# Kernel optimization log

Measured on AMD Instinct MI355X. Metric: run time of the kernel, lower is better.

The kernel has to match this reference:

```python
import jax, jax.numpy as jnp
import numpy as np

EMBED = 1024
HEADS = 16
HDIM = 64
FF = 4096
N, S = 2, 2048
EPS = 1e-5


def _ln(x, g, b):
    m = jnp.mean(x, axis=-1, keepdims=True)
    v = jnp.mean((x - m) ** 2, axis=-1, keepdims=True)
    return (x - m) / jnp.sqrt(v + EPS) * g + b


def setup_inputs() -> dict:
    key = jax.random.key(0)
    ks = jax.random.split(key, 12)
    sd = 0.02
    inp = {
        'x': jax.random.normal(ks[0], (N, S, EMBED), dtype=jnp.float32),
        'mask': jnp.ones((N, 1, S, S), dtype=jnp.int32),
        'Wq': jax.random.normal(ks[1], (EMBED, HEADS * HDIM), dtype=jnp.float32) * sd,
        'bq': jnp.zeros((HEADS * HDIM,), dtype=jnp.float32),
        'Wk': jax.random.normal(ks[2], (EMBED, HEADS * HDIM), dtype=jnp.float32) * sd,
        'bk': jnp.zeros((HEADS * HDIM,), dtype=jnp.float32),
        'Wv': jax.random.normal(ks[3], (EMBED, HEADS * HDIM), dtype=jnp.float32) * sd,
        'bv': jnp.zeros((HEADS * HDIM,), dtype=jnp.float32),
        'Wo': jax.random.normal(ks[4], (HEADS * HDIM, EMBED), dtype=jnp.float32) * sd,
        'bo': jnp.zeros((EMBED,), dtype=jnp.float32),
        'g1': jnp.ones((EMBED,), dtype=jnp.float32),
        'beta1': jnp.zeros((EMBED,), dtype=jnp.float32),
        'g2': jnp.ones((EMBED,), dtype=jnp.float32),
        'beta2': jnp.zeros((EMBED,), dtype=jnp.float32),
        'W1': jax.random.normal(ks[5], (EMBED, FF), dtype=jnp.float32) * sd,
        'b1': jnp.zeros((FF,), dtype=jnp.float32),
        'W2': jax.random.normal(ks[6], (FF, EMBED), dtype=jnp.float32) * sd,
        'b2': jnp.zeros((EMBED,), dtype=jnp.float32),
    }
    return inp


def reference(x, mask, Wq, bq, Wk, bk, Wv, bv, Wo, bo, g1, beta1, g2, beta2, W1, b1, W2, b2):
    n, q_len, _ = x.shape
    # QKV projections, split into heads: [n, s, h, d]
    Q = (x @ Wq + bq).reshape(n, q_len, HEADS, HDIM)
    K = (x @ Wk + bk).reshape(n, q_len, HEADS, HDIM)
    V = (x @ Wv + bv).reshape(n, q_len, HEADS, HDIM)
    scores = jnp.einsum('nqhd,nkhd->nhqk', Q, K)
    scores = jnp.where(mask == 0, -jnp.inf, scores)
    # NOTE: original torch code is `attention / embed_size ** 1 / 2`,
    # which parses as (scores / embed_size) / 2 — replicated faithfully.
    attn = jax.nn.softmax(scores / EMBED / 2.0, axis=-1)
    ctx = jnp.einsum('nhqk,nkhd->nqhd', attn, V).reshape(n, q_len, HEADS * HDIM)
    proj = ctx @ Wo + bo
    h = _ln(proj + x, g1, beta1)  # dropout is identity (eval / p=0)
    ff = jax.nn.relu(h @ W1 + b1) @ W2 + b2
    out = _ln(ff + h, g2, beta2)
    return out
```

## Files before the change

### kernel.cpp

```cpp
#include <hip/hip_runtime.h>
#include <hip/hip_bf16.h>
#include <cstdint>
#include <cstddef>

#define EMBED 1024
#define SLEN  2048
#define NB    2
#define HEADS 16
#define HDIM  64
#define FFDIM 4096
#define ROWS  (NB * SLEN)
#define LOG2E 1.4426950408889634f

typedef __attribute__((ext_vector_type(8))) __bf16 bf16x8;
typedef __attribute__((ext_vector_type(4))) __bf16 bf16x4;
typedef __attribute__((ext_vector_type(4))) float  f32x4;

__device__ __forceinline__ void gload_lds16(const void* g, void* l) {
  __builtin_amdgcn_global_load_lds(
      (const __attribute__((address_space(1))) void*)g,
      (__attribute__((address_space(3))) void*)l, 16, 0, 0);
}

#define BAR()                              \
  do {                                     \
    __builtin_amdgcn_s_barrier();          \
    __builtin_amdgcn_sched_barrier(0);     \
  } while (0)
#define WAITVM(N)                                           \
  do {                                                      \
    asm volatile("s_waitcnt vmcnt(" #N ")" ::: "memory");   \
  } while (0)

__global__ __launch_bounds__(256) void cast_f32_bf16(const float* __restrict__ in,
                                                     __bf16* __restrict__ out, int n4) {
  int i = blockIdx.x * 256 + threadIdx.x;
  if (i >= n4) return;
  float4 v = ((const float4*)in)[i];
  bf16x4 o;
  o.x = (__bf16)v.x; o.y = (__bf16)v.y; o.z = (__bf16)v.z; o.w = (__bf16)v.w;
  ((bf16x4*)out)[i] = o;
}

__global__ __launch_bounds__(256) void transpose_all(
    const float* __restrict__ Wq, const float* __restrict__ Wk,
    const float* __restrict__ Wv, const float* __restrict__ Wo,
    const float* __restrict__ W1, const float* __restrict__ W2,
    __bf16* __restrict__ Wqt, __bf16* __restrict__ Wkt, __bf16* __restrict__ Wvt,
    __bf16* __restrict__ Wot, __bf16* __restrict__ W1t, __bf16* __restrict__ W2t) {
  __shared__ float t[64][65];
  const int b = blockIdx.x;
  const float* src;
  __bf16* dst;
  int R, C, tile;
  if (b < 1024) {
    const int w = b >> 8;
    tile = b & 255; R = 1024; C = 1024;
    src = (w == 0) ? Wq : (w == 1) ? Wk : (w == 2) ? Wv : Wo;
    dst = (w == 0) ? Wqt : (w == 1) ? Wkt : (w == 2) ? Wvt : Wot;
  } else if (b < 2048) {
    tile = b - 1024; R = 1024; C = 4096; src = W1; dst = W1t;
  } else {
    tile = b - 2048; R = 4096; C = 1024; src = W2; dst = W2t;
  }
  const int ct = C >> 6;
  const int tr = (tile / ct) * 64, tc = (tile % ct) * 64;
  const int tx = threadIdx.x & 63;
  const int ty = threadIdx.x >> 6;
#pragma unroll
  for (int i = 0; i < 16; ++i) {
    int a = ty * 16 + i;
    t[a][tx] = src[(size_t)(tr + a) * C + tc + tx];
  }
  __syncthreads();
#pragma unroll
  for (int i = 0; i < 16; ++i) {
    int bb = ty * 16 + i;
    dst[(size_t)(tc + bb) * R + tr + tx] = (__bf16)t[tx][bb];
  }
}

__global__ __launch_bounds__(256) void mask_flags_k(const int* __restrict__ mask,
                                                    int* __restrict__ flags) {
  const int b = blockIdx.x;
  const int kt = b & 31, qt = (b >> 5) & 15, n = b >> 9;
  const int tid = threadIdx.x;
  const int* base = mask + ((size_t)n * SLEN + qt * 128) * SLEN + kt * 64;
  const int rw = tid >> 4;
  const int cg = tid & 15;
  int ok = 1;
#pragma unroll
  for (int i = 0; i < 8; ++i) {
    int4 v = ((const int4*)(base + (size_t)(rw + i * 16) * SLEN))[cg];
    ok &= (v.x != 0) & (v.y != 0) & (v.z != 0) & (v.w != 0);
  }
  __shared__ int red;
  if (tid == 0) red = 1;
  __syncthreads();
  if (!ok) red = 0;
  __syncthreads();
  if (tid == 0) flags[b] = red;
}

template <int MODE>
__global__ __launch_bounds__(512, 1) void gemm256(
    const __bf16* __restrict__ A, const __bf16* __restrict__ Bt,
    const float* __restrict__ bias, const float* __restrict__ bias2,
    const float* __restrict__ bias3,
    void* __restrict__ outp, void* __restrict__ outp2, void* __restrict__ outp3,
    int M, int N, int K, int Kc, float oscale) {
  __shared__ __align__(16) char smem[69632];
  const int tid = threadIdx.x;
  const int lane = tid & 63;
  const int ntile = N >> 8;
  const int mt = M >> 8;
  const int cpx = gridDim.x >> 3;
  int u = (blockIdx.x & 7) * cpx + (blockIdx.x >> 3);
  int kz = 0;
  if constexpr (MODE == 5) {
    const int tiles = mt * ntile;
    kz = u / tiles;
    u -= kz * tiles;
  }
  int bm, bn;
  {
    const int G = (ntile >= 4) ? 4 : ntile;
    const int gsz = mt * G;
    const int g = u / gsz;
    const int rem = u - g * gsz;
    bm = rem / G;
    bn = g * G + rem % G;
  }
  const int trow = bm << 8, tcol = bn << 8;

  const int r0 = tid & 255;
  const int c0 = tid >> 8;
  const __bf16* Ag = A + (size_t)(trow + r0) * K + (size_t)kz * Kc + c0 * 8;
  const __bf16* Bg = Bt + (size_t)(tcol + r0) * K + (size_t)kz * Kc + c0 * 8;

  auto stage = [&](int buf, int kt) {
    const __bf16* a0 = Ag + (size_t)kt * 32;
    const __bf16* b0 = Bg + (size_t)kt * 32;
    char* la = smem + buf * 32768 + tid * 16;
    char* lb = la + 16384;
    gload_lds16(a0, la);
    gload_lds16(a0 + 16, la + 8192);
    gload_lds16(b0, lb);
    gload_lds16(b0 + 16, lb + 8192);
  };

  const int wave = tid >> 6;
  const int wr = wave >> 2;
  const int wc = wave & 3;
  const int l16 = lane & 15;
  const int g4 = lane >> 4;

  f32x4 acc[8][4];
#pragma unroll
  for (int i = 0; i < 8; ++i)
#pragma unroll
    for (int j = 0; j < 4; ++j) acc[i][j] = (f32x4)0.0f;

  const int nk = Kc >> 5;
  stage(0, 0);
  stage(1, 1);
  WAITVM(4);
  BAR();
  int cur = 0;
  for (int kt = 0; kt < nk; ++kt) {
    bf16x8 af[8], bfr[4];
#pragma unroll
    for (int i = 0; i < 8; ++i)
      af[i] = *(const bf16x8*)(smem + cur * 32768 + g4 * 4096 +
                               (wr * 128 + i * 16 + l16) * 16);
#pragma unroll
    for (int j = 0; j < 4; ++j)
      bfr[j] = *(const bf16x8*)(smem + cur * 32768 + 16384 + g4 * 4096 +
                                (wc * 64 + j * 16 + l16) * 16);
#pragma unroll
    for (int mi = 0; mi < 8; ++mi)
#pragma unroll
      for (int ni = 0; ni < 4; ++ni)
        acc[mi][ni] =
            __builtin_amdgcn_mfma_f32_16x16x32_bf16(af[mi], bfr[ni], acc[mi][ni], 0, 0, 0);
    BAR();
    if (kt + 2 < nk) {
      stage(cur, kt + 2);
      WAITVM(4);
    } else {
      WAITVM(0);
    }
    BAR();
    cur ^= 1;
  }

  if constexpr (MODE == 5) {
#pragma unroll
    for (int mi = 0; mi < 8; ++mi)
#pragma unroll
      for (int ni = 0; ni < 4; ++ni) {
        const int col = tcol + wc * 64 + ni * 16 + l16;
#pragma unroll
        for (int r = 0; r < 4; ++r) {
          const int row = trow + wr * 128 + mi * 16 + g4 * 4 + r;
          ((float*)outp)[(size_t)kz * M * N + (size_t)row * N + col] = acc[mi][ni][r];
        }
      }
  } else {
    const int sel = (MODE == 4) ? (tcol >> 10) : 0;
    const float* bp = (MODE == 4) ? (sel == 0 ? bias : sel == 1 ? bias2 : bias3) : bias;
    const int cc0 = (MODE == 4) ? (tcol & 1023) : tcol;
    const int n = trow >> 11;
    if (MODE == 4 && sel == 2) {
      __bf16(*repT)[136] = (__bf16(*)[136])smem;
#pragma unroll
      for (int h = 0; h < 2; ++h) {
        __syncthreads();
        if (wr == h) {
#pragma unroll
          for (int mi = 0; mi < 8; ++mi)
#pragma unroll
            for (int ni = 0; ni < 4; ++ni) {
              const int cl = wc * 64 + ni * 16 + l16;
              const float bcol = bp[cc0 + cl];
#pragma unroll
              for (int r = 0; r < 4; ++r)
                repT[cl][mi * 16 + g4 * 4 + r] = (__bf16)(acc[mi][ni][r] + bcol);
            }
        }
        __syncthreads();
#pragma unroll
        for (int it = 0; it < 8; ++it) {
          const int cidx = it * 512 + tid;
          const int cl = cidx >> 4, seg = cidx & 15;
          const int col = cc0 + cl, hh = col >> 6, dd = col & 63;
          *(bf16x8*)((__bf16*)outp3 + ((size_t)((n * HEADS + hh) * HDIM) + dd) * SLEN +
                     (trow & 2047) + h * 128 + seg * 8) = *(const bf16x8*)&repT[cl][seg * 8];
        }
      }
    } else {
      __bf16(*rep)[264] = (__bf16(*)[264])smem;
#pragma unroll
      for (int h = 0; h < 2; ++h) {
        __syncthreads();
        if (wr == h) {
#pragma unroll
          for (int mi = 0; mi < 8; ++mi)
#pragma unroll
            for (int ni = 0; ni < 4; ++ni) {
              const int cl = wc * 64 + ni * 16 + l16;
              float bcol = bp[cc0 + cl];
#pragma unroll
              for (int r = 0; r < 4; ++r) {
                float v = acc[mi][ni][r] + bcol;
                if constexpr (MODE == 4) {
                  if (sel == 0) v *= oscale;
                } else {
                  v = fmaxf(v, 0.0f);
                }
                rep[mi * 16 + g4 * 4 + r][cl] = (__bf16)v;
              }
            }
        }
        __syncthreads();
        if constexpr (MODE == 3) {
#pragma unroll
          for (int it = 0; it < 8; ++it) {
            const int cidx = it * 512 + tid;
            const int rl = cidx >> 5, seg = cidx & 31;
            *(bf16x8*)((__bf16*)outp + (size_t)(trow + h * 128 + rl) * N + tcol + seg * 8) =
                *(const bf16x8*)&rep[rl][seg * 8];
          }
        } else {
          __bf16* dst = (sel == 0) ? (__bf16*)outp : (__bf16*)outp2;
#pragma unroll
          for (int it = 0; it < 8; ++it) {
            const int cidx = it * 512 + tid;
            const int rl = cidx >> 5, seg = cidx & 31;
            const int col = cc0 + seg * 8, hh = col >> 6, d = col & 63;
            const int s = (trow & 2047) + h * 128 + rl;
            *(bf16x8*)(dst + ((size_t)((n * HEADS + hh) * SLEN) + s) * HDIM + d) =
                *(const bf16x8*)&rep[rl][seg * 8];
          }
        }
      }
    }
  }
}

__global__ __launch_bounds__(256, 2) void gemm_bt5(
    const __bf16* __restrict__ A, const __bf16* __restrict__ Bt,
    float* __restrict__ outp, int M, int N, int K, int Kc) {
  __shared__ __align__(16) char smem[32768];
  const int tid = threadIdx.x;
  const int lane = tid & 63;
  const int ntile = N >> 7;
  const int cpx = gridDim.x >> 3;
  int u = (blockIdx.x & 7) * cpx + (blockIdx.x >> 3);
  const int tiles = (M >> 7) * ntile;
  const int kz = u / tiles;
  u -= kz * tiles;
  const int bm = u / ntile;
  const int bn = u % ntile;
  const int trow = bm << 7;
  const int tcol = bn << 7;

  const int c0 = tid >> 7;
  const int r0 = tid & 127;
  const __bf16* Ag = A + (size_t)(trow + r0) * K + (size_t)kz * Kc + c0 * 8;
  const __bf16* Bg = Bt + (size_t)(tcol + r0) * K + (size_t)kz * Kc + c0 * 8;

  auto stage = [&](int buf, int kt) {
    const __bf16* a0 = Ag + (size_t)kt * 32;
    const __bf16* b0 = Bg + (size_t)kt * 32;
    char* la = smem + buf * 16384 + tid * 16;
    char* lb = la + 8192;
    gload_lds16(a0, la);
    gload_lds16(a0 + 16, la + 4096);
    gload_lds16(b0, lb);
    gload_lds16(b0 + 16, lb + 4096);
  };

  const int wave = tid >> 6;
  const int wr = (wave >> 1) * 64;
  const int wc = (wave & 1) * 64;
  const int l16 = lane & 15;
  const int g4 = lane >> 4;

  f32x4 acc[4][4];
#pragma unroll
  for (int i = 0; i < 4; ++i)
#pragma unroll
    for (int j = 0; j < 4; ++j) acc[i][j] = (f32x4)0.0f;

  const int nk = Kc >> 5;
  stage(0, 0);
  stage(1, 1);
  WAITVM(4);
  BAR();
  int cur = 0;
  for (int kt = 0; kt < nk; ++kt) {
    bf16x8 af[4], bfr[4];
#pragma unroll
    for (int i = 0; i < 4; ++i) {
      af[i]  = *(const bf16x8*)(smem + cur * 16384 + g4 * 2048 + (wr + i * 16 + l16) * 16);
      bfr[i] = *(const bf16x8*)(smem + cur * 16384 + 8192 + g4 * 2048 + (wc + i * 16 + l16) * 16);
    }
#pragma unroll
    for (int mi = 0; mi < 4; ++mi)
#pragma unroll
      for (int ni = 0; ni < 4; ++ni)
        acc[mi][ni] =
            __builtin_amdgcn_mfma_f32_16x16x32_bf16(af[mi], bfr[ni], acc[mi][ni], 0, 0, 0);
    BAR();
    if (kt + 2 < nk) {
      stage(cur, kt + 2);
      WAITVM(4);
    } else {
      WAITVM(0);
    }
    BAR();
    cur ^= 1;
  }
#pragma unroll
  for (int mi = 0; mi < 4; ++mi)
#pragma unroll
    for (int ni = 0; ni < 4; ++ni) {
      const int col = tcol + wc + ni * 16 + l16;
#pragma unroll
      for (int r = 0; r < 4; ++r) {
        const int row = trow + wr + mi * 16 + g4 * 4 + r;
        outp[(size_t)kz * M * N + (size_t)row * N + col] = acc[mi][ni][r];
      }
    }
}

__global__ __launch_bounds__(256, 3) void attn_k(const __bf16* __restrict__ Q,
                                                 const __bf16* __restrict__ K,
                                                 const __bf16* __restrict__ Vt,
                                                 const int* __restrict__ mask,
                                                 const int* __restrict__ flags,
                                                 __bf16* __restrict__ ctx) {
  const int tid = threadIdx.x, lane = tid & 63, wave = tid >> 6;
  const int l16 = lane & 15, g4 = lane >> 4;
  const int bid = blockIdx.x;
  const int lb = (bid & 7) * 64 + (bid >> 3);
  const int qt = lb & 15, h = (lb >> 4) & 15, n = lb >> 8;
  const int q0 = qt * 128 + wave * 32;
  const __bf16* Qh = Q + (size_t)(n * HEADS + h) * SLEN * HDIM;
  const __bf16* Kh = K + (size_t)(n * HEADS + h) * SLEN * HDIM;
  const __bf16* Vh = Vt + (size_t)(n * HEADS + h) * HDIM * SLEN;
  const int* Mh = mask + (size_t)n * SLEN * SLEN;
  const int* Fh = flags + (n * 16 + qt) * 32;

  __shared__ __bf16 KV[2][2][8][64][8];
  __shared__ __align__(16) __bf16 P_lds[4][2][16][72];

  const int srow = tid & 63;
  const int schunk = tid >> 6;
  const __bf16* Kg = Kh + (size_t)srow * HDIM + schunk * 8;
  const __bf16* Vg = Vh + (size_t)srow * SLEN + schunk * 8;
  auto stage = [&](int buf, int kb) {
    char* lk = (char*)&KV[buf][0][0][0][0] + tid * 16;
    char* lv = (char*)&KV[buf][1][0][0][0] + tid * 16;
    const __bf16* kg = Kg + (size_t)kb * 64 * HDIM;
    const __bf16* vg = Vg + kb * 64;
    gload_lds16(kg, lk);
    gload_lds16(kg + 32, lk + 4096);
    gload_lds16(vg, lv);
    gload_lds16(vg + 32, lv + 4096);
  };

  const unsigned long long fbits = __ballot(Fh[lane & 31] != 0);

  bf16x8 qf[2][2];
#pragma unroll
  for (int mq = 0; mq < 2; ++mq)
#pragma unroll
    for (int kd = 0; kd < 2; ++kd)
      qf[mq][kd] =
          *(const bf16x8*)(Qh + (size_t)(q0 + mq * 16 + l16) * HDIM + kd * 32 + g4 * 8);

  float m_[2], lsum[2];
  f32x4 o[2][4];
#pragma unroll
  for (int mq = 0; mq < 2; ++mq) {
    m_[mq] = -INFINITY;
    lsum[mq] = 0.0f;
#pragma unroll
    for (int ni = 0; ni < 4; ++ni) o[mq][ni] = (f32x4)0.0f;
  }

  const int nt = SLEN / 64;
  stage(0, 0);
  stage(1, 1);
  WAITVM(4);
  BAR();
  int cur = 0;
  for (int kt = 0; kt < nt; ++kt) {
    const int kbase = kt * 64;
    const bool full = (fbits >> kt) & 1ull;
    f32x4 s[2][4];
#pragma unroll
    for (int mq = 0; mq < 2; ++mq)
#pragma unroll
      for (int ni = 0; ni < 4; ++ni) s[mq][ni] = (f32x4)0.0f;
    __builtin_amdgcn_s_setprio(1);
#pragma unroll
    for (int ni = 0; ni < 4; ++ni) {
      bf16x8 kf0 = *(const bf16x8*)&KV[cur][0][g4][ni * 16 + l16][0];
      bf16x8 kf1 = *(const bf16x8*)&KV[cur][0][4 + g4][ni * 16 + l16][0];
#pragma unroll
      for (int mq = 0; mq < 2; ++mq) {
        s[mq][ni] = __builtin_amdgcn_mfma_f32_16x16x32_bf16(kf0, qf[mq][0], s[mq][ni], 0, 0, 0);
        s[mq][ni] = __builtin_amdgcn_mfma_f32_16x16x32_bf16(kf1, qf[mq][1], s[mq][ni], 0, 0, 0);
      }
    }
    __builtin_amdgcn_s_setprio(0);
    if (!full) {
#pragma unroll
      for (int mq = 0; mq < 2; ++mq)
#pragma unroll
        for (int ni = 0; ni < 4; ++ni)
#pragma unroll
          for (int r = 0; r < 4; ++r) {
            const int mk =
                Mh[(size_t)(q0 + mq * 16 + l16) * SLEN + kbase + ni * 16 + 4 * g4 + r];
            s[mq][ni][r] = mk ? s[mq][ni][r] : -INFINITY;
          }
    }
    float pmax[2];
#pragma unroll
    for (int mq = 0; mq < 2; ++mq) {
      float a = fmaxf(fmaxf(s[mq][0][0], s[mq][0][1]), fmaxf(s[mq][0][2], s[mq][0][3]));
      float b = fmaxf(fmaxf(s[mq][1][0], s[mq][1][1]), fmaxf(s[mq][1][2], s[mq][1][3]));
      float c = fmaxf(fmaxf(s[mq][2][0], s[mq][2][1]), fmaxf(s[mq][2][2], s[mq][2][3]));
      float d = fmaxf(fmaxf(s[mq][3][0], s[mq][3][1]), fmaxf(s[mq][3][2], s[mq][3][3]));
      pmax[mq] = fmaxf(fmaxf(a, b), fmaxf(c, d));
    }
    const int ok = (pmax[0] <= m_[0] + 8.0f) & (pmax[1] <= m_[1] + 8.0f);
    if (!__all(ok)) {
#pragma unroll
      for (int mq = 0; mq < 2; ++mq) {
        float pm = fmaxf(m_[mq], pmax[mq]);
        pm = fmaxf(pm, __shfl_xor(pm, 16));
        pm = fmaxf(pm, __shfl_xor(pm, 32));
        const float al = __builtin_amdgcn_exp2f(m_[mq] - pm);
        m_[mq] = pm;
        lsum[mq] *= al;
#pragma unroll
        for (int r = 0; r < 4; ++r) {
          const float ao = __shfl(al, 4 * g4 + r);
#pragma unroll
          for (int ni = 0; ni < 4; ++ni) o[mq][ni][r] *= ao;
        }
      }
    }
#pragma unroll
    for (int mq = 0; mq < 2; ++mq) {
      float ls = 0.0f;
#pragma unroll
      for (int ni = 0; ni < 4; ++ni) {
        bf16x4 pk;
#pragma unroll
        for (int r = 0; r < 4; ++r) {
          const float p = __builtin_amdgcn_exp2f(s[mq][ni][r] - m_[mq]);
          ls += p;
          pk[r] = (__bf16)p;
        }
        *(bf16x4*)&P_lds[wave][mq][l16][ni * 16 + 4 * g4] = pk;
      }
      lsum[mq] += ls;
    }
    __builtin_amdgcn_s_setprio(1);
#pragma unroll
    for (int kb = 0; kb < 2; ++kb) {
      bf16x8 pa0 = *(const bf16x8*)&P_lds[wave][0][l16][kb * 32 + 8 * g4];
      bf16x8 pa1 = *(const bf16x8*)&P_lds[wave][1][l16][kb * 32 + 8 * g4];
#pragma unroll
      for (int ni = 0; ni < 4; ++ni) {
        bf16x8 vf = *(const bf16x8*)&KV[cur][1][kb * 4 + g4][ni * 16 + l16][0];
        o[0][ni] = __builtin_amdgcn_mfma_f32_16x16x32_bf16(pa0, vf, o[0][ni], 0, 0, 0);
        o[1][ni] = __builtin_amdgcn_mfma_f32_16x16x32_bf16(pa1, vf, o[1][ni], 0, 0, 0);
      }
    }
    __builtin_amdgcn_s_setprio(0);
    BAR();
    if (kt + 2 < nt) {
      stage(cur, kt + 2);
      WAITVM(4);
    } else {
      WAITVM(0);
    }
    BAR();
    cur ^= 1;
  }
#pragma unroll
  for (int mq = 0; mq < 2; ++mq) {
    float l = lsum[mq];
    l += __shfl_xor(l, 16);
    l += __shfl_xor(l, 32);
    lsum[mq] = l;
  }
#pragma unroll
  for (int mq = 0; mq < 2; ++mq) {
#pragma unroll
    for (int r = 0; r < 4; ++r) {
      const float inv = __builtin_amdgcn_rcpf(__shfl(lsum[mq], 4 * g4 + r));
#pragma unroll
      for (int ni = 0; ni < 4; ++ni) {
        ctx[((size_t)(n * SLEN) + q0 + mq * 16 + 4 * g4 + r) * EMBED + h * HDIM + ni * 16 +
            l16] = (__bf16)(o[mq][ni][r] * inv);
      }
    }
  }
}

__global__ __launch_bounds__(256) void ln_fused_k(const float* __restrict__ p, int nz,
                                                  const float* __restrict__ bias,
                                                  const float* __restrict__ res,
                                                  const float* __restrict__ gw,
                                                  const float* __restrict__ bw,
                                                  float* __restrict__ of,
                                                  __bf16* __restrict__ ob) {
  const int tid = threadIdx.x;
  const size_t row = blockIdx.x;
  float4 bb = ((const float4*)bias)[tid];
  float4 rr = ((const float4*)(res + row * EMBED))[tid];
  float4 v;
  v.x = bb.x + rr.x; v.y = bb.y + rr.y; v.z = bb.z + rr.z; v.w = bb.w + rr.w;
  for (int z = 0; z < nz; ++z) {
    float4 pz = ((const float4*)(p + (size_t)z * ROWS * EMBED + row * EMBED))[tid];
    v.x += pz.x; v.y += pz.y; v.z += pz.z; v.w += pz.w;
  }
  float s = v.x + v.y + v.z + v.w;
  float sq = v.x * v.x + v.y * v.y + v.z * v.z + v.w * v.w;
#pragma unroll
  for (int off = 1; off < 64; off <<= 1) {
    s += __shfl_xor(s, off);
    sq += __shfl_xor(sq, off);
  }
  __shared__ float red[8];
  if ((tid & 63) == 0) { red[tid >> 6] = s; red[4 + (tid >> 6)] = sq; }
  __syncthreads();
  s = red[0] + red[1] + red[2] + red[3];
  sq = red[4] + red[5] + red[6] + red[7];
  const float mean = s * (1.0f / EMBED);
  const float var = sq * (1.0f / EMBED) - mean * mean;
  const float rstd = rsqrtf(var + 1e-5f);
  float4 gv = ((const float4*)gw)[tid];
  float4 bv2 = ((const float4*)bw)[tid];
  float4 ov;
  ov.x = (v.x - mean) * rstd * gv.x + bv2.x;
  ov.y = (v.y - mean) * rstd * gv.y + bv2.y;
  ov.z = (v.z - mean) * rstd * gv.z + bv2.z;
  ov.w = (v.w - mean) * rstd * gv.w + bv2.w;
  ((float4*)(of + row * EMBED))[tid] = ov;
  if (ob) {
    bf16x4 oh;
    oh.x = (__bf16)ov.x; oh.y = (__bf16)ov.y; oh.z = (__bf16)ov.z; oh.w = (__bf16)ov.w;
    ((bf16x4*)(ob + row * EMBED))[tid] = oh;
  }
}

extern "C" void kernel_launch(void* const* d_in, const int* in_sizes, int n_in,
                              void* d_out, int out_size, void* d_ws, size_t ws_size,
                              hipStream_t stream) {
  (void)in_sizes; (void)n_in; (void)out_size;
  const float* x   = (const float*)d_in[0];
  const int*  mask = (const int*)d_in[1];
  const float* Wq = (const float*)d_in[2];  const float* bq  = (const float*)d_in[3];
  const float* Wk = (const float*)d_in[4];  const float* bk  = (const float*)d_in[5];
  const float* Wv = (const float*)d_in[6];  const float* bv  = (const float*)d_in[7];
  const float* Wo = (const float*)d_in[8];  const float* bo  = (const float*)d_in[9];
  const float* g1 = (const float*)d_in[10]; const float* be1 = (const float*)d_in[11];
  const float* g2 = (const float*)d_in[12]; const float* be2 = (const float*)d_in[13];
  const float* W1 = (const float*)d_in[14]; const float* b1  = (const float*)d_in[15];
  const float* W2 = (const float*)d_in[16]; const float* b2  = (const float*)d_in[17];

  char* ws = (char*)d_ws;
  size_t off = 0;
  auto alloc = [&](size_t bytes) -> void* {
    void* p = ws + off;
    off += (bytes + 255) & ~(size_t)255;
    return p;
  };
  __bf16* xb   = (__bf16*)alloc((size_t)ROWS * EMBED * 2);
  __bf16* Wqt  = (__bf16*)alloc((size_t)EMBED * EMBED * 2);
  __bf16* Wkt  = (__bf16*)alloc((size_t)EMBED * EMBED * 2);
  __bf16* Wvt  = (__bf16*)alloc((size_t)EMBED * EMBED * 2);
  __bf16* Wot  = (__bf16*)alloc((size_t)EMBED * EMBED * 2);
  __bf16* W1t  = (__bf16*)alloc((size_t)EMBED * FFDIM * 2);
  __bf16* W2t  = (__bf16*)alloc((size_t)FFDIM * EMBED * 2);
  __bf16* Qb   = (__bf16*)alloc((size_t)ROWS * EMBED * 2);
  __bf16* Kb   = (__bf16*)alloc((size_t)ROWS * EMBED * 2);
  __bf16* Vtb  = (__bf16*)alloc((size_t)ROWS * EMBED * 2);
  __bf16* ctxb = (__bf16*)alloc((size_t)ROWS * EMBED * 2);
  float* hf     = (float*)alloc((size_t)ROWS * EMBED * 4);
  __bf16* hb    = (__bf16*)alloc((size_t)ROWS * EMBED * 2);
  __bf16* a1    = (__bf16*)alloc((size_t)ROWS * FFDIM * 2);
  int*   mflags = (int*)alloc(NB * 16 * 32 * sizeof(int));

  const size_t pneed = (size_t)4 * ROWS * EMBED * sizeof(float);
  int kspF2;
  float* pF2;
  if (off + pneed <= ws_size) {
    pF2 = (float*)alloc(pneed);
    kspF2 = 4;
  } else {
    pF2 = (float*)Qb;
    kspF2 = 2;
  }
  float* pWo = (float*)a1;

  cast_f32_bf16<<<ROWS * EMBED / 4 / 256, 256, 0, stream>>>(x, xb, ROWS * EMBED / 4);
  transpose_all<<<3072, 256, 0, stream>>>(Wq, Wk, Wv, Wo, W1, W2,
                                          Wqt, Wkt, Wvt, Wot, W1t, W2t);
  mask_flags_k<<<NB * 16 * 32, 256, 0, stream>>>(mask, mflags);

  gemm256<4><<<(ROWS / 256) * (3 * EMBED / 256), 512, 0, stream>>>(
      xb, Wqt, bq, bk, bv, Qb, Kb, Vtb, ROWS, 3 * EMBED, EMBED, EMBED, LOG2E / 2048.0f);
  attn_k<<<NB * HEADS * (SLEN / 128), 256, 0, stream>>>(Qb, Kb, Vtb, mask, mflags, ctxb);
  gemm_bt5<<<(ROWS / 128) * (EMBED / 128) * 2, 256, 0, stream>>>(
      ctxb, Wot, pWo, ROWS, EMBED, EMBED, EMBED / 2);
  ln_fused_k<<<ROWS, 256, 0, stream>>>(pWo, 2, bo, x, g1, be1, hf, hb);
  gemm256<3><<<(ROWS / 256) * (FFDIM / 256), 512, 0, stream>>>(
      hb, W1t, b1, nullptr, nullptr, a1, nullptr, nullptr, ROWS, FFDIM, EMBED, EMBED, 1.0f);
  gemm256<5><<<(ROWS / 256) * (EMBED / 256) * kspF2, 512, 0, stream>>>(
      a1, W2t, nullptr, nullptr, nullptr, pF2, nullptr, nullptr,
      ROWS, EMBED, FFDIM, FFDIM / kspF2, 1.0f);
  ln_fused_k<<<ROWS, 256, 0, stream>>>(pF2, kspF2, b2, hf, g2, be2, (float*)d_out, nullptr);
}
```

Measured before the change: 311.6 us.

## Split attention over two key halves with combine pass; triple-buffer GEMM LDS

The attention kernel now runs twice as many blocks, each covering half the key range. It writes unnormalised partial outputs plus per-row max and sum, and a new combine kernel merges the two halves into ctx. This is meant to fill more CUs, since there were only 512 attention blocks before. Separately, both GEMM kernels move from double to triple-buffered LDS staging to hide load latency, which uses more shared memory and raises gemm_bt5's launch bound to 3 blocks per SM. The cost is an extra kernel launch, bf16 rounding of the partial outputs, and higher LDS use.

```diff
diff --git a/kernel.cpp b/kernel.cpp
--- a/kernel.cpp
+++ b/kernel.cpp
@@ -109,7 +109,7 @@
     const float* __restrict__ bias3,
     void* __restrict__ outp, void* __restrict__ outp2, void* __restrict__ outp3,
     int M, int N, int K, int Kc, float oscale) {
-  __shared__ __align__(16) char smem[69632];
+  __shared__ __align__(16) char smem[98304];
   const int tid = threadIdx.x;
   const int lane = tid & 63;
   const int ntile = N >> 8;
@@ -164,7 +164,8 @@
   const int nk = Kc >> 5;
   stage(0, 0);
   stage(1, 1);
-  WAITVM(4);
+  stage(2, 2);
+  WAITVM(8);
   BAR();
   int cur = 0;
   for (int kt = 0; kt < nk; ++kt) {
@@ -184,14 +185,16 @@
         acc[mi][ni] =
             __builtin_amdgcn_mfma_f32_16x16x32_bf16(af[mi], bfr[ni], acc[mi][ni], 0, 0, 0);
     BAR();
-    if (kt + 2 < nk) {
-      stage(cur, kt + 2);
+    if (kt + 3 < nk) {
+      stage(cur, kt + 3);
+      WAITVM(8);
+    } else if (kt + 3 == nk) {
       WAITVM(4);
     } else {
       WAITVM(0);
     }
     BAR();
-    cur ^= 1;
+    cur = (cur == 2) ? 0 : cur + 1;
   }
 
   if constexpr (MODE == 5) {
@@ -288,10 +291,10 @@
   }
 }
 
-__global__ __launch_bounds__(256, 2) void gemm_bt5(
+__global__ __launch_bounds__(256, 3) void gemm_bt5(
     const __bf16* __restrict__ A, const __bf16* __restrict__ Bt,
     float* __restrict__ outp, int M, int N, int K, int Kc) {
-  __shared__ __align__(16) char smem[32768];
+  __shared__ __align__(16) char smem[49152];
   const int tid = threadIdx.x;
   const int lane = tid & 63;
   const int ntile = N >> 7;
@@ -336,7 +339,8 @@
   const int nk = Kc >> 5;
   stage(0, 0);
   stage(1, 1);
-  WAITVM(4);
+  stage(2, 2);
+  WAITVM(8);
   BAR();
   int cur = 0;
   for (int kt = 0; kt < nk; ++kt) {
@@ -353,14 +357,16 @@
         acc[mi][ni] =
             __builtin_amdgcn_mfma_f32_16x16x32_bf16(af[mi], bfr[ni], acc[mi][ni], 0, 0, 0);
     BAR();
-    if (kt + 2 < nk) {
-      stage(cur, kt + 2);
+    if (kt + 3 < nk) {
+      stage(cur, kt + 3);
+      WAITVM(8);
+    } else if (kt + 3 == nk) {
       WAITVM(4);
     } else {
       WAITVM(0);
     }
     BAR();
-    cur ^= 1;
+    cur = (cur == 2) ? 0 : cur + 1;
   }
 #pragma unroll
   for (int mi = 0; mi < 4; ++mi)
@@ -380,13 +386,18 @@
                                                  const __bf16* __restrict__ Vt,
                                                  const int* __restrict__ mask,
                                                  const int* __restrict__ flags,
-                                                 __bf16* __restrict__ ctx) {
+                                                 __bf16* __restrict__ po,
+                                                 float* __restrict__ pm,
+                                                 float* __restrict__ pl) {
   const int tid = threadIdx.x, lane = tid & 63, wave = tid >> 6;
   const int l16 = lane & 15, g4 = lane >> 4;
   const int bid = blockIdx.x;
-  const int lb = (bid & 7) * 64 + (bid >> 3);
-  const int qt = lb & 15, h = (lb >> 4) & 15, n = lb >> 8;
+  const int lb = (bid & 7) * 128 + (bid >> 3);
+  const int half = lb & 1;
+  const int v = lb >> 1;
+  const int qt = v & 15, h = (v >> 4) & 15, n = v >> 8;
   const int q0 = qt * 128 + wave * 32;
+  const int k0 = half * 16;
   const __bf16* Qh = Q + (size_t)(n * HEADS + h) * SLEN * HDIM;
   const __bf16* Kh = K + (size_t)(n * HEADS + h) * SLEN * HDIM;
   const __bf16* Vh = Vt + (size_t)(n * HEADS + h) * HDIM * SLEN;
@@ -431,13 +442,13 @@
     for (int ni = 0; ni < 4; ++ni) o[mq][ni] = (f32x4)0.0f;
   }
 
-  const int nt = SLEN / 64;
-  stage(0, 0);
-  stage(1, 1);
+  const int kend = k0 + 16;
+  stage(0, k0);
+  stage(1, k0 + 1);
   WAITVM(4);
   BAR();
   int cur = 0;
-  for (int kt = 0; kt < nt; ++kt) {
+  for (int kt = k0; kt < kend; ++kt) {
     const int kbase = kt * 64;
     const bool full = (fbits >> kt) & 1ull;
     f32x4 s[2][4];
@@ -482,11 +493,11 @@
     if (!__all(ok)) {
 #pragma unroll
       for (int mq = 0; mq < 2; ++mq) {
-        float pm = fmaxf(m_[mq], pmax[mq]);
-        pm = fmaxf(pm, __shfl_xor(pm, 16));
-        pm = fmaxf(pm, __shfl_xor(pm, 32));
-        const float al = __builtin_amdgcn_exp2f(m_[mq] - pm);
-        m_[mq] = pm;
+        float pm2 = fmaxf(m_[mq], pmax[mq]);
+        pm2 = fmaxf(pm2, __shfl_xor(pm2, 16));
+        pm2 = fmaxf(pm2, __shfl_xor(pm2, 32));
+        const float al = __builtin_amdgcn_exp2f(m_[mq] - pm2);
+        m_[mq] = pm2;
         lsum[mq] *= al;
 #pragma unroll
         for (int r = 0; r < 4; ++r) {
@@ -526,7 +537,7 @@
     }
     __builtin_amdgcn_s_setprio(0);
     BAR();
-    if (kt + 2 < nt) {
+    if (kt + 2 < kend) {
       stage(cur, kt + 2);
       WAITVM(4);
     } else {
@@ -542,17 +553,54 @@
     l += __shfl_xor(l, 32);
     lsum[mq] = l;
   }
+  const size_t pidx = (size_t)half * 512 + ((n * HEADS + h) * 16 + qt);
 #pragma unroll
   for (int mq = 0; mq < 2; ++mq) {
 #pragma unroll
     for (int r = 0; r < 4; ++r) {
-      const float inv = __builtin_amdgcn_rcpf(__shfl(lsum[mq], 4 * g4 + r));
-#pragma unroll
-      for (int ni = 0; ni < 4; ++ni) {
-        ctx[((size_t)(n * SLEN) + q0 + mq * 16 + 4 * g4 + r) * EMBED + h * HDIM + ni * 16 +
-            l16] = (__bf16)(o[mq][ni][r] * inv);
-      }
-    }
+      const int ql = wave * 32 + mq * 16 + 4 * g4 + r;
+#pragma unroll
+      for (int ni = 0; ni < 4; ++ni)
+        po[(pidx * 128 + ql) * 64 + ni * 16 + l16] = (__bf16)o[mq][ni][r];
+    }
+    if (g4 == 0) {
+      const int ql = wave * 32 + mq * 16 + l16;
+      pm[pidx * 128 + ql] = m_[mq];
+      pl[pidx * 128 + ql] = lsum[mq];
+    }
+  }
+}
+
+__global__ __launch_bounds__(256) void attn_combine(const __bf16* __restrict__ po,
+                                                    const float* __restrict__ pm,
+                                                    const float* __restrict__ pl,
+                                                    __bf16* __restrict__ ctx) {
+  const int idx = blockIdx.x;
+  const int tid = threadIdx.x;
+  const int q = tid >> 1;
+  const int dh = (tid & 1) * 32;
+  const int n = idx >> 8, h = (idx >> 4) & 15, qt = idx & 15;
+  const float m0 = pm[(size_t)idx * 128 + q];
+  const float m1 = pm[(size_t)(512 + idx) * 128 + q];
+  const float l0 = pl[(size_t)idx * 128 + q];
+  const float l1 = pl[(size_t)(512 + idx) * 128 + q];
+  const float m = fmaxf(m0, m1);
+  const float s0 = __builtin_amdgcn_exp2f(m0 - m);
+  const float s1 = __builtin_amdgcn_exp2f(m1 - m);
+  const float inv = 1.0f / (l0 * s0 + l1 * s1);
+  const float f0 = s0 * inv, f1 = s1 * inv;
+  const __bf16* o0 = po + ((size_t)idx * 128 + q) * 64 + dh;
+  const __bf16* o1 = po + ((size_t)(512 + idx) * 128 + q) * 64 + dh;
+  __bf16* dst = ctx + ((size_t)(n * SLEN) + qt * 128 + q) * EMBED + h * HDIM + dh;
+#pragma unroll
+  for (int j = 0; j < 4; ++j) {
+    bf16x8 v0 = ((const bf16x8*)o0)[j];
+    bf16x8 v1 = ((const bf16x8*)o1)[j];
+    bf16x8 w;
+#pragma unroll
+    for (int e = 0; e < 8; ++e)
+      w[e] = (__bf16)((float)v0[e] * f0 + (float)v1[e] * f1);
+    ((bf16x8*)dst)[j] = w;
   }
 }
 
@@ -652,6 +700,9 @@
     kspF2 = 2;
   }
   float* pWo = (float*)a1;
+  __bf16* po = (__bf16*)hf;
+  float*  pm = (float*)hb;
+  float*  pl = pm + 2 * 512 * 128;
 
   cast_f32_bf16<<<ROWS * EMBED / 4 / 256, 256, 0, stream>>>(x, xb, ROWS * EMBED / 4);
   transpose_all<<<3072, 256, 0, stream>>>(Wq, Wk, Wv, Wo, W1, W2,
@@ -660,7 +711,9 @@
 
   gemm256<4><<<(ROWS / 256) * (3 * EMBED / 256), 512, 0, stream>>>(
       xb, Wqt, bq, bk, bv, Qb, Kb, Vtb, ROWS, 3 * EMBED, EMBED, EMBED, LOG2E / 2048.0f);
-  attn_k<<<NB * HEADS * (SLEN / 128), 256, 0, stream>>>(Qb, Kb, Vtb, mask, mflags, ctxb);
+  attn_k<<<NB * HEADS * (SLEN / 128) * 2, 256, 0, stream>>>(Qb, Kb, Vtb, mask, mflags,
+                                                            po, pm, pl);
+  attn_combine<<<NB * HEADS * (SLEN / 128), 256, 0, stream>>>(po, pm, pl, ctxb);
   gemm_bt5<<<(ROWS / 128) * (EMBED / 128) * 2, 256, 0, stream>>>(
       ctxb, Wot, pWo, ROWS, EMBED, EMBED, EMBED / 2);
   ln_fused_k<<<ROWS, 256, 0, stream>>>(pWo, 2, bo, x, g1, be1, hf, hb);
```

After: 318.3 us. 1.02x slower.

## Deepen GEMM LDS pipelines to four stages and prefetch attention K/V fragments

Applied to the files above, without the earlier changes.

Both GEMM kernels move from a double-buffered LDS scheme to a four-slot ring with three tiles in flight. The next global-to-LDS stage is issued before the MFMAs, and each iteration now needs one barrier instead of two. The main GEMM also splits its A-fragment LDS reads so the first MFMA half can start while the second half of the fragments is still loading. The attention kernel hoists all K and V fragment reads to the top of each iteration with explicit lgkmcnt waits and moves the next-stage issue after a single barrier. The larger LDS allocation (128KB for gemm256, 64KB per block for gemm_bt5) can reduce occupancy, and the new scheme relies on hand-written waitcnt accounting.

```diff
diff --git a/kernel.cpp b/kernel.cpp
--- a/kernel.cpp
+++ b/kernel.cpp
@@ -22,6 +22,7 @@
       (__attribute__((address_space(3))) void*)l, 16, 0, 0);
 }
 
+#define SCHED() __builtin_amdgcn_sched_barrier(0)
 #define BAR()                              \
   do {                                     \
     __builtin_amdgcn_s_barrier();          \
@@ -30,6 +31,10 @@
 #define WAITVM(N)                                           \
   do {                                                      \
     asm volatile("s_waitcnt vmcnt(" #N ")" ::: "memory");   \
+  } while (0)
+#define WAITLGKM(N)                                         \
+  do {                                                      \
+    asm volatile("s_waitcnt lgkmcnt(" #N ")" ::: "memory"); \
   } while (0)
 
 __global__ __launch_bounds__(256) void cast_f32_bf16(const float* __restrict__ in,
@@ -109,7 +114,7 @@
     const float* __restrict__ bias3,
     void* __restrict__ outp, void* __restrict__ outp2, void* __restrict__ outp3,
     int M, int N, int K, int Kc, float oscale) {
-  __shared__ __align__(16) char smem[69632];
+  __shared__ __align__(16) char smem[131072];
   const int tid = threadIdx.x;
   const int lane = tid & 63;
   const int ntile = N >> 8;
@@ -164,34 +169,54 @@
   const int nk = Kc >> 5;
   stage(0, 0);
   stage(1, 1);
-  WAITVM(4);
+  stage(2, 2);
+  WAITVM(8);
   BAR();
-  int cur = 0;
   for (int kt = 0; kt < nk; ++kt) {
+    const int cur = kt & 3;
+    const char* base = smem + cur * 32768;
     bf16x8 af[8], bfr[4];
 #pragma unroll
-    for (int i = 0; i < 8; ++i)
-      af[i] = *(const bf16x8*)(smem + cur * 32768 + g4 * 4096 +
-                               (wr * 128 + i * 16 + l16) * 16);
+    for (int i = 0; i < 4; ++i)
+      af[i] = *(const bf16x8*)(base + g4 * 4096 + (wr * 128 + i * 16 + l16) * 16);
 #pragma unroll
     for (int j = 0; j < 4; ++j)
-      bfr[j] = *(const bf16x8*)(smem + cur * 32768 + 16384 + g4 * 4096 +
-                                (wc * 64 + j * 16 + l16) * 16);
-#pragma unroll
-    for (int mi = 0; mi < 8; ++mi)
+      bfr[j] = *(const bf16x8*)(base + 16384 + g4 * 4096 + (wc * 64 + j * 16 + l16) * 16);
+    SCHED();
+#pragma unroll
+    for (int i = 4; i < 8; ++i)
+      af[i] = *(const bf16x8*)(base + g4 * 4096 + (wr * 128 + i * 16 + l16) * 16);
+    if (kt + 3 < nk) stage((kt + 3) & 3, kt + 3);
+    SCHED();
+    WAITLGKM(4);
+    SCHED();
+    __builtin_amdgcn_s_setprio(1);
+#pragma unroll
+    for (int mi = 0; mi < 4; ++mi)
 #pragma unroll
       for (int ni = 0; ni < 4; ++ni)
         acc[mi][ni] =
             __builtin_amdgcn_mfma_f32_16x16x32_bf16(af[mi], bfr[ni], acc[mi][ni], 0, 0, 0);
+    __builtin_amdgcn_s_setprio(0);
+    SCHED();
+    WAITLGKM(0);
+    SCHED();
+    __builtin_amdgcn_s_setprio(1);
+#pragma unroll
+    for (int mi = 4; mi < 8; ++mi)
+#pragma unroll
+      for (int ni = 0; ni < 4; ++ni)
+        acc[mi][ni] =
+            __builtin_amdgcn_mfma_f32_16x16x32_bf16(af[mi], bfr[ni], acc[mi][ni], 0, 0, 0);
+    __builtin_amdgcn_s_setprio(0);
+    if (kt + 3 < nk) {
+      WAITVM(8);
+    } else if (kt + 3 == nk) {
+      WAITVM(4);
+    } else if (kt + 2 == nk) {
+      WAITVM(0);
+    }
     BAR();
-    if (kt + 2 < nk) {
-      stage(cur, kt + 2);
-      WAITVM(4);
-    } else {
-      WAITVM(0);
-    }
-    BAR();
-    cur ^= 1;
   }
 
   if constexpr (MODE == 5) {
@@ -291,7 +316,7 @@
 __global__ __launch_bounds__(256, 2) void gemm_bt5(
     const __bf16* __restrict__ A, const __bf16* __restrict__ Bt,
     float* __restrict__ outp, int M, int N, int K, int Kc) {
-  __shared__ __align__(16) char smem[32768];
+  __shared__ __align__(16) char smem[65536];
   const int tid = threadIdx.x;
   const int lane = tid & 63;
   const int ntile = N >> 7;
@@ -336,31 +361,38 @@
   const int nk = Kc >> 5;
   stage(0, 0);
   stage(1, 1);
-  WAITVM(4);
+  stage(2, 2);
+  WAITVM(8);
   BAR();
-  int cur = 0;
   for (int kt = 0; kt < nk; ++kt) {
+    const int cur = kt & 3;
+    const char* base = smem + cur * 16384;
     bf16x8 af[4], bfr[4];
 #pragma unroll
     for (int i = 0; i < 4; ++i) {
-      af[i]  = *(const bf16x8*)(smem + cur * 16384 + g4 * 2048 + (wr + i * 16 + l16) * 16);
-      bfr[i] = *(const bf16x8*)(smem + cur * 16384 + 8192 + g4 * 2048 + (wc + i * 16 + l16) * 16);
-    }
+      af[i]  = *(const bf16x8*)(base + g4 * 2048 + (wr + i * 16 + l16) * 16);
+      bfr[i] = *(const bf16x8*)(base + 8192 + g4 * 2048 + (wc + i * 16 + l16) * 16);
+    }
+    if (kt + 3 < nk) stage((kt + 3) & 3, kt + 3);
+    SCHED();
+    WAITLGKM(0);
+    SCHED();
+    __builtin_amdgcn_s_setprio(1);
 #pragma unroll
     for (int mi = 0; mi < 4; ++mi)
 #pragma unroll
       for (int ni = 0; ni < 4; ++ni)
         acc[mi][ni] =
             __builtin_amdgcn_mfma_f32_16x16x32_bf16(af[mi], bfr[ni], acc[mi][ni], 0, 0, 0);
+    __builtin_amdgcn_s_setprio(0);
+    if (kt + 3 < nk) {
+      WAITVM(8);
+    } else if (kt + 3 == nk) {
+      WAITVM(4);
+    } else if (kt + 2 == nk) {
+      WAITVM(0);
+    }
     BAR();
-    if (kt + 2 < nk) {
-      stage(cur, kt + 2);
-      WAITVM(4);
-    } else {
-      WAITVM(0);
-    }
-    BAR();
-    cur ^= 1;
   }
 #pragma unroll
   for (int mi = 0; mi < 4; ++mi)
@@ -440,6 +472,21 @@
   for (int kt = 0; kt < nt; ++kt) {
     const int kbase = kt * 64;
     const bool full = (fbits >> kt) & 1ull;
+    bf16x8 kf[4][2], vf[2][4];
+#pragma unroll
+    for (int ni = 0; ni < 4; ++ni) {
+      kf[ni][0] = *(const bf16x8*)&KV[cur][0][g4][ni * 16 + l16][0];
+      kf[ni][1] = *(const bf16x8*)&KV[cur][0][4 + g4][ni * 16 + l16][0];
+    }
+    SCHED();
+#pragma unroll
+    for (int kb = 0; kb < 2; ++kb)
+#pragma unroll
+      for (int ni = 0; ni < 4; ++ni)
+        vf[kb][ni] = *(const bf16x8*)&KV[cur][1][kb * 4 + g4][ni * 16 + l16][0];
+    SCHED();
+    WAITLGKM(8);
+    SCHED();
     f32x4 s[2][4];
 #pragma unroll
     for (int mq = 0; mq < 2; ++mq)
@@ -447,15 +494,12 @@
       for (int ni = 0; ni < 4; ++ni) s[mq][ni] = (f32x4)0.0f;
     __builtin_amdgcn_s_setprio(1);
 #pragma unroll
-    for (int ni = 0; ni < 4; ++ni) {
-      bf16x8 kf0 = *(const bf16x8*)&KV[cur][0][g4][ni * 16 + l16][0];
-      bf16x8 kf1 = *(const bf16x8*)&KV[cur][0][4 + g4][ni * 16 + l16][0];
+    for (int ni = 0; ni < 4; ++ni)
 #pragma unroll
       for (int mq = 0; mq < 2; ++mq) {
-        s[mq][ni] = __builtin_amdgcn_mfma_f32_16x16x32_bf16(kf0, qf[mq][0], s[mq][ni], 0, 0, 0);
-        s[mq][ni] = __builtin_amdgcn_mfma_f32_16x16x32_bf16(kf1, qf[mq][1], s[mq][ni], 0, 0, 0);
-      }
-    }
+        s[mq][ni] = __builtin_amdgcn_mfma_f32_16x16x32_bf16(kf[ni][0], qf[mq][0], s[mq][ni], 0, 0, 0);
+        s[mq][ni] = __builtin_amdgcn_mfma_f32_16x16x32_bf16(kf[ni][1], qf[mq][1], s[mq][ni], 0, 0, 0);
+      }
     __builtin_amdgcn_s_setprio(0);
     if (!full) {
 #pragma unroll
@@ -482,11 +526,11 @@
     if (!__all(ok)) {
 #pragma unroll
       for (int mq = 0; mq < 2; ++mq) {
-        float pm = fmaxf(m_[mq], pmax[mq]);
-        pm = fmaxf(pm, __shfl_xor(pm, 16));
-        pm = fmaxf(pm, __shfl_xor(pm, 32));
-        const float al = __builtin_amdgcn_exp2f(m_[mq] - pm);
-        m_[mq] = pm;
+        float pm2 = fmaxf(m_[mq], pmax[mq]);
+        pm2 = fmaxf(pm2, __shfl_xor(pm2, 16));
+        pm2 = fmaxf(pm2, __shfl_xor(pm2, 32));
+        const float al = __builtin_amdgcn_exp2f(m_[mq] - pm2);
+        m_[mq] = pm2;
         lsum[mq] *= al;
 #pragma unroll
         for (int r = 0; r < 4; ++r) {
@@ -512,27 +556,27 @@
       }
       lsum[mq] += ls;
     }
+    bf16x8 pa[2][2];
+#pragma unroll
+    for (int kb = 0; kb < 2; ++kb) {
+      pa[0][kb] = *(const bf16x8*)&P_lds[wave][0][l16][kb * 32 + 8 * g4];
+      pa[1][kb] = *(const bf16x8*)&P_lds[wave][1][l16][kb * 32 + 8 * g4];
+    }
+    SCHED();
+    WAITLGKM(0);
+    SCHED();
     __builtin_amdgcn_s_setprio(1);
 #pragma unroll
-    for (int kb = 0; kb < 2; ++kb) {
-      bf16x8 pa0 = *(const bf16x8*)&P_lds[wave][0][l16][kb * 32 + 8 * g4];
-      bf16x8 pa1 = *(const bf16x8*)&P_lds[wave][1][l16][kb * 32 + 8 * g4];
+    for (int kb = 0; kb < 2; ++kb)
 #pragma unroll
       for (int ni = 0; ni < 4; ++ni) {
-        bf16x8 vf = *(const bf16x8*)&KV[cur][1][kb * 4 + g4][ni * 16 + l16][0];
-        o[0][ni] = __builtin_amdgcn_mfma_f32_16x16x32_bf16(pa0, vf, o[0][ni], 0, 0, 0);
-        o[1][ni] = __builtin_amdgcn_mfma_f32_16x16x32_bf16(pa1, vf, o[1][ni], 0, 0, 0);
-      }
-    }
+        o[0][ni] = __builtin_amdgcn_mfma_f32_16x16x32_bf16(pa[0][kb], vf[kb][ni], o[0][ni], 0, 0, 0);
+        o[1][ni] = __builtin_amdgcn_mfma_f32_16x16x32_bf16(pa[1][kb], vf[kb][ni], o[1][ni], 0, 0, 0);
+      }
     __builtin_amdgcn_s_setprio(0);
+    WAITVM(0);
     BAR();
-    if (kt + 2 < nt) {
-      stage(cur, kt + 2);
-      WAITVM(4);
-    } else {
-      WAITVM(0);
-    }
-    BAR();
+    if (kt + 2 < nt) stage(cur, kt + 2);
     cur ^= 1;
   }
 #pragma unroll
```

New measurement: 289.5 us. -7.1%, faster.
